# Kernel optimization log

Measured on AMD Instinct MI355X. Metric: run time of the kernel, lower is better.

## Reference

```python
import jax, jax.numpy as jnp
import numpy as np

B, S, D = 4, 2048, 1024
H, HD = 16, 64  # n_heads, head_dim; D == H*HD


def setup_inputs() -> dict:
    key = jax.random.key(0)
    k1, k2, k3, k4, k5 = jax.random.split(key, 5)
    s = 0.02
    return {
        "x": jax.random.normal(k1, (B, S, D), dtype=jnp.float32),
        "w_qkv": jax.random.normal(k2, (D, 3 * D), dtype=jnp.float32) * s,
        "b_qkv": jax.random.normal(k3, (3 * D,), dtype=jnp.float32) * s,
        "w_out": jax.random.normal(k4, (D, D), dtype=jnp.float32) * s,
        "b_out": jax.random.normal(k5, (D,), dtype=jnp.float32) * s,
    }


def reference(x, w_qkv, b_qkv, w_out, b_out):
    b, s, d = x.shape
    qkv = x @ w_qkv + b_qkv                      # [B,S,3D]
    qkv = qkv.reshape(b, s, 3, H, HD)
    qkv = jnp.transpose(qkv, (2, 0, 3, 1, 4))    # [3,B,H,S,HD]
    q, k, v = qkv[0], qkv[1], qkv[2]
    scale = 1.0 / np.sqrt(HD).astype(np.float32)
    scores = jnp.einsum("bhqd,bhkd->bhqk", q, k) * scale  # [B,H,S,S]
    causal = jnp.tril(jnp.ones((s, s), dtype=bool))
    scores = jnp.where(causal[None, None], scores, -jnp.inf)
    weights = jax.nn.softmax(scores, axis=-1)
    attn = jnp.einsum("bhqk,bhkd->bhqd", weights, v)       # [B,H,S,HD]
    attn = jnp.transpose(attn, (0, 2, 1, 3)).reshape(b, s, d)
    return attn @ w_out + b_out
```

## Files before the change

kernel.cpp:

```cpp
#include <hip/hip_runtime.h>
#include <hip/hip_bf16.h>

#define B_DIM 4
#define S_DIM 2048
#define D_DIM 1024
#define H_DIM 16
#define HD_DIM 64

using bf16 = __hip_bfloat16;
using bf16x8 = __attribute__((ext_vector_type(8))) short;
using f32x4 = __attribute__((ext_vector_type(4))) float;

__device__ inline unsigned short f2bfu(float f) {
    bf16 h = __float2bfloat16(f);
    unsigned short s;
    __builtin_memcpy(&s, &h, 2);
    return s;
}
__device__ inline unsigned int pack2bf(float a, float b) {
    return (unsigned int)f2bfu(a) | ((unsigned int)f2bfu(b) << 16);
}
__device__ inline float exp2_raw(float x) {
    float r;
    asm("v_exp_f32 %0, %1" : "=v"(r) : "v"(x));
    return r;
}

typedef __attribute__((address_space(1))) const void cg_void;
typedef __attribute__((address_space(3))) void lds_void;
__device__ inline void gload_lds16(const void* g, void* l) {
    __builtin_amdgcn_global_load_lds((cg_void*)g, (lds_void*)l, 16, 0, 0);
}

__global__ __launch_bounds__(256) void prep_kernel(const float* __restrict__ x,
                                                   bf16* __restrict__ xb,
                                                   const float* __restrict__ wq,
                                                   bf16* __restrict__ wqT,
                                                   const float* __restrict__ wo,
                                                   bf16* __restrict__ woT) {
    int bid = blockIdx.x;
    int tid = threadIdx.x;
    if (bid < 8192) {
        int i = bid * 256 + tid;
        float4 v = reinterpret_cast<const float4*>(x)[i];
        ushort4 o;
        o.x = f2bfu(v.x); o.y = f2bfu(v.y); o.z = f2bfu(v.z); o.w = f2bfu(v.w);
        reinterpret_cast<ushort4*>(xb)[i] = o;
        return;
    }
    __shared__ float tile[32][33];
    const float* in;
    bf16* out;
    int R, C, bx, by;
    if (bid < 11264) {
        int loc = bid - 8192;
        in = wq; out = wqT; R = D_DIM; C = 3 * D_DIM;
        bx = loc % 96; by = loc / 96;
    } else {
        int loc = bid - 11264;
        in = wo; out = woT; R = D_DIM; C = D_DIM;
        bx = loc % 32; by = loc / 32;
    }
    int tx = tid & 31, ty = tid >> 5;
    int c0 = bx * 32, r0 = by * 32;
#pragma unroll
    for (int i = 0; i < 32; i += 8)
        tile[ty + i][tx] = in[(size_t)(r0 + ty + i) * C + c0 + tx];
    __syncthreads();
#pragma unroll
    for (int i = 0; i < 32; i += 8)
        out[(size_t)(c0 + ty + i) * R + r0 + tx] = __float2bfloat16(tile[tx][ty + i]);
}

#define GEMM_PREAMBLE()                                                        \
    const int K = D_DIM;                                                       \
    __shared__ __align__(16) char smem[65536];                                 \
    int bid3 = blockIdx.x;                                                     \
    int xcd = bid3 & 7;                                                        \
    int inner = bid3 >> 3;                                                     \
    int m0 = ((xcd << 3) | (inner & 7)) * 128;        \
    int n0 = (inner >> 3) * 128;                              \
    int tid = threadIdx.x;                                                     \
    int lane = tid & 63;                                                       \
    int w = tid >> 6;                                                          \
    int wr = w >> 1, wc = w & 1;                                               \
    int lr = lane & 15, lk = lane >> 4;                                        \
    f32x4 acc[4][4] = {};                                                      \
    int sr8 = lane >> 3;                                     \
    int scol = (((lane & 7) * 16) ^ (sr8 << 4)) >> 1;    \
    int wub = w * 1024;                                                        \
    const int rsw = (lr & 7) << 4;                                             \
    const bf16* Arow = A + (size_t)(m0 + w * 8 + sr8) * K + scol;              \
    const bf16* Brow = BT + (size_t)(n0 + w * 8 + sr8) * K + scol;

#define GEMM_STAGE_A(buf, kk)                                                  \
    do {                                                                       \
        char* aa_ = smem + (buf) * 32768;                                      \
        gload_lds16(Arow + (kk), aa_ + wub);                                   \
        gload_lds16(Arow + 32 * 1024 + (kk), aa_ + 4096 + wub);                \
        gload_lds16(Arow + 64 * 1024 + (kk), aa_ + 8192 + wub);                \
        gload_lds16(Arow + 96 * 1024 + (kk), aa_ + 12288 + wub);               \
    } while (0)

#define GEMM_STAGE_B(buf, kk)                                                  \
    do {                                                                       \
        char* bb_ = smem + (buf) * 32768 + 16384;                              \
        gload_lds16(Brow + (kk), bb_ + wub);                                   \
        gload_lds16(Brow + 32 * 1024 + (kk), bb_ + 4096 + wub);                \
        gload_lds16(Brow + 64 * 1024 + (kk), bb_ + 8192 + wub);                \
        gload_lds16(Brow + 96 * 1024 + (kk), bb_ + 12288 + wub);               \
    } while (0)

#define GEMM_MAINLOOP()                                                        \
    const int NT = K / 64;                                             \
    GEMM_STAGE_B(0, 0);                                                        \
    GEMM_STAGE_A(0, 0);                                                        \
    bf16x8 af0[4], af1[4], bf0[4], bf1[4], pa1[4], pb1[4];                     \
    for (int t = 0; t < NT; ++t) {                                             \
        char* as = smem + (t & 1) * 32768;                                     \
        char* bs = as + 16384;                                                 \
              \
        asm volatile("s_waitcnt vmcnt(4)" ::: "memory");                       \
        __builtin_amdgcn_s_barrier();                                          \
        __builtin_amdgcn_sched_barrier(0);                                     \
        _Pragma("unroll")                                                      \
        for (int n = 0; n < 4; ++n) {                                          \
            int rb = (wc * 64 + n * 16 + lr) * 128;                            \
            bf0[n] = *(const bf16x8*)(bs + rb + ((lk * 16) ^ rsw));            \
            bf1[n] = *(const bf16x8*)(bs + rb + ((64 + lk * 16) ^ rsw));       \
        }                                                                      \
        if (t + 1 < NT) GEMM_STAGE_B((t + 1) & 1, (t + 1) * 64);               \
        if (t) {                                                               \
            __builtin_amdgcn_s_setprio(1);                                     \
            _Pragma("unroll")                                                  \
            for (int m = 0; m < 4; ++m)                                        \
                _Pragma("unroll")                                              \
                for (int n = 0; n < 4; ++n)                                    \
                    acc[m][n] = __builtin_amdgcn_mfma_f32_16x16x32_bf16(       \
                        pa1[m], pb1[n], acc[m][n], 0, 0, 0);                   \
            __builtin_amdgcn_s_setprio(0);                                     \
        }                                                                      \
                \
        if (t + 1 < NT) asm volatile("s_waitcnt vmcnt(4)" ::: "memory");       \
        else            asm volatile("s_waitcnt vmcnt(0)" ::: "memory");       \
        __builtin_amdgcn_s_barrier();                                          \
        __builtin_amdgcn_sched_barrier(0);                                     \
        _Pragma("unroll")                                                      \
        for (int m = 0; m < 4; ++m) {                                          \
            int rb = (wr * 64 + m * 16 + lr) * 128;                            \
            af0[m] = *(const bf16x8*)(as + rb + ((lk * 16) ^ rsw));            \
            af1[m] = *(const bf16x8*)(as + rb + ((64 + lk * 16) ^ rsw));       \
        }                                                                      \
        if (t + 1 < NT) GEMM_STAGE_A((t + 1) & 1, (t + 1) * 64);               \
        __builtin_amdgcn_s_setprio(1);                                         \
        _Pragma("unroll")                                                      \
        for (int m = 0; m < 4; ++m)                                            \
            _Pragma("unroll")                                                  \
            for (int n = 0; n < 4; ++n)                                        \
                acc[m][n] = __builtin_amdgcn_mfma_f32_16x16x32_bf16(           \
                    af0[m], bf0[n], acc[m][n], 0, 0, 0);                       \
        __builtin_amdgcn_s_setprio(0);                                         \
        _Pragma("unroll")                                                      \
        for (int m = 0; m < 4; ++m) pa1[m] = af1[m];                           \
        _Pragma("unroll")                                                      \
        for (int n = 0; n < 4; ++n) pb1[n] = bf1[n];                           \
    }                                                                          \
                                              \
    _Pragma("unroll")                                                          \
    for (int m = 0; m < 4; ++m)                                                \
        _Pragma("unroll")                                                      \
        for (int n = 0; n < 4; ++n)                                            \
            acc[m][n] = __builtin_amdgcn_mfma_f32_16x16x32_bf16(               \
                pa1[m], pb1[n], acc[m][n], 0, 0, 0);

__global__ __launch_bounds__(256, 2) void gemm_qkv_kernel(const bf16* __restrict__ A,
                                                          const bf16* __restrict__ BT,
                                                          const float* __restrict__ bias,
                                                          bf16* __restrict__ Qo,
                                                          bf16* __restrict__ Ko,
                                                          bf16* __restrict__ Vt) {
    GEMM_PREAMBLE();
    GEMM_MAINLOOP();
    const float QS = 0.18033688f;
    int third = n0 >> 10;
#pragma unroll
    for (int m = 0; m < 4; ++m) {
        int row = m0 + wr * 64 + m * 16 + lk * 4;
        int b = row >> 11, s = row & 2047;
#pragma unroll
        for (int n = 0; n < 4; ++n) {
            int col = n0 + wc * 64 + n * 16 + lr;
            int rem = col & 1023;
            int h = rem >> 6, hd = rem & 63;
            float bv = bias[col];
            if (third == 0) {
#pragma unroll
                for (int i = 0; i < 4; ++i)
                    Qo[(((size_t)b * H_DIM + h) * S_DIM + s + i) * HD_DIM + hd] =
                        __float2bfloat16((acc[m][n][i] + bv) * QS);
            } else if (third == 1) {
#pragma unroll
                for (int i = 0; i < 4; ++i)
                    Ko[(((size_t)b * H_DIM + h) * S_DIM + s + i) * HD_DIM + hd] =
                        __float2bfloat16(acc[m][n][i] + bv);
            } else {
                uint2 d;
                d.x = pack2bf(acc[m][n][0] + bv, acc[m][n][1] + bv);
                d.y = pack2bf(acc[m][n][2] + bv, acc[m][n][3] + bv);
                *(uint2*)&Vt[(((size_t)b * H_DIM + h) * HD_DIM + hd) * S_DIM + s] = d;
            }
        }
    }
}

__global__ __launch_bounds__(256, 4) void attn_kernel(const bf16* __restrict__ Q,
                                                      const bf16* __restrict__ K,
                                                      const bf16* __restrict__ Vt,
                                                      bf16* __restrict__ Aout) {
    __shared__ __align__(16) char smem[40960];
    int bid = blockIdx.x;
    int bh = bid & 63;
    const int st_tbl[16] = {15, 14, 13, 12, 8, 9, 10, 11, 4, 5, 6, 7, 3, 2, 1, 0};
    int st = st_tbl[bid >> 6];
    int b = bh >> 4, h = bh & 15;
    int w = threadIdx.x >> 6;
    int lane = threadIdx.x & 63;
    int lr = lane & 15, lk = lane >> 4;

    const short* Qs = (const short*)(Q + (size_t)bh * S_DIM * HD_DIM);
    const short* Ks = (const short*)(K + (size_t)bh * S_DIM * HD_DIM);
    const short* Vs = (const short*)(Vt + (size_t)bh * HD_DIM * S_DIM);
    char* pb = smem + 32768 + w * 2048;
    const int sw = (lr & 7) << 4;

    int srow = w * 8 + (lane >> 3);
    int sblk = ((lane & 7) ^ (lane >> 3)) * 8;
    int wub = w * 1024;

    int q0w = st * 128 + w * 32;
    int nt = 2 * st + 2;
    int twl = 2 * st + ((w >> 1) & 1);

    bf16x8 qf[2][2];
#pragma unroll
    for (int qg = 0; qg < 2; ++qg)
#pragma unroll
        for (int c = 0; c < 2; ++c)
            qf[qg][c] = *(const bf16x8*)&Qs[(size_t)(q0w + qg * 16 + lr) * 64 + c * 32 + lk * 8];

    bf16x8 onesv;
#pragma unroll
    for (int z = 0; z < 8; ++z) onesv[z] = (short)0x3F80;

    f32x4 o[4][2] = {};
    f32x4 ol[2] = {};

    gload_lds16(Ks + (size_t)srow * 64 + sblk, smem + wub);
    gload_lds16(Ks + (size_t)(32 + srow) * 64 + sblk, smem + 4096 + wub);
    gload_lds16(Vs + (size_t)srow * S_DIM + sblk, smem + 16384 + wub);
    gload_lds16(Vs + (size_t)(32 + srow) * S_DIM + sblk, smem + 20480 + wub);

    for (int t = 0; t < nt; ++t) {
        int cur = t & 1;
        int kv0 = t * 64;
        __syncthreads();
        if (t + 1 < nt) {
            int kn = kv0 + 64;
            char* kd = smem + (cur ^ 1) * 8192;
            char* vd = smem + 16384 + (cur ^ 1) * 8192;
            gload_lds16(Ks + (size_t)(kn + srow) * 64 + sblk, kd + wub);
            gload_lds16(Ks + (size_t)(kn + 32 + srow) * 64 + sblk, kd + 4096 + wub);
            gload_lds16(Vs + (size_t)srow * S_DIM + kn + sblk, vd + wub);
            gload_lds16(Vs + (size_t)(32 + srow) * S_DIM + kn + sblk, vd + 4096 + wub);
        }
        if (t > twl) continue;
        char* kt = smem + cur * 8192;
        char* vt = smem + 16384 + cur * 8192;
        bool diag = (t == twl);
        int mhi = diag ? ((w & 1) ? 4 : 2) : 4;

        f32x4 s[4][2] = {};
        __builtin_amdgcn_s_setprio(1);
#pragma unroll
        for (int m = 0; m < 4; ++m) {
            if (m >= mhi) continue;
            int rb = (m * 16 + lr) * 128;
            bf16x8 ka = *(const bf16x8*)(kt + rb + ((lk * 16) ^ sw));
            bf16x8 kb2 = *(const bf16x8*)(kt + rb + ((64 + lk * 16) ^ sw));
            s[m][0] = __builtin_amdgcn_mfma_f32_16x16x32_bf16(ka, qf[0][0], s[m][0], 0, 0, 0);
            s[m][0] = __builtin_amdgcn_mfma_f32_16x16x32_bf16(kb2, qf[0][1], s[m][0], 0, 0, 0);
            s[m][1] = __builtin_amdgcn_mfma_f32_16x16x32_bf16(ka, qf[1][0], s[m][1], 0, 0, 0);
            s[m][1] = __builtin_amdgcn_mfma_f32_16x16x32_bf16(kb2, qf[1][1], s[m][1], 0, 0, 0);
        }
        __builtin_amdgcn_s_setprio(0);

        if (kv0 + 63 > q0w) {
#pragma unroll
            for (int m = 0; m < 4; ++m)
#pragma unroll
                for (int qg = 0; qg < 2; ++qg) {
                    int qq = q0w + qg * 16 + lr;
#pragma unroll
                    for (int i = 0; i < 4; ++i)
                        if (kv0 + m * 16 + lk * 4 + i > qq) s[m][qg][i] = -1e30f;
                }
        }

#pragma unroll
        for (int m = 0; m < 4; ++m)
#pragma unroll
            for (int qg = 0; qg < 2; ++qg)
#pragma unroll
                for (int i = 0; i < 4; ++i) s[m][qg][i] = exp2_raw(s[m][qg][i]);

        bf16x8 pf[2][2];
#pragma unroll
        for (int qg = 0; qg < 2; ++qg) {
#pragma unroll
            for (int m = 0; m < 4; ++m) {
                uint2 d;
                d.x = pack2bf(s[m][qg][0], s[m][qg][1]);
                d.y = pack2bf(s[m][qg][2], s[m][qg][3]);
                *(uint2*)(pb + lr * 128 + ((m * 32 + lk * 8) ^ sw)) = d;
            }
            pf[qg][0] = *(const bf16x8*)(pb + lr * 128 + ((lk * 16) ^ sw));
            pf[qg][1] = *(const bf16x8*)(pb + lr * 128 + ((64 + lk * 16) ^ sw));
        }

        __builtin_amdgcn_s_setprio(1);
#pragma unroll
        for (int m = 0; m < 4; ++m) {
            int rb = (m * 16 + lr) * 128;
            bf16x8 va = *(const bf16x8*)(vt + rb + ((lk * 16) ^ sw));
            bf16x8 vb2 = *(const bf16x8*)(vt + rb + ((64 + lk * 16) ^ sw));
            o[m][0] = __builtin_amdgcn_mfma_f32_16x16x32_bf16(va, pf[0][0], o[m][0], 0, 0, 0);
            o[m][0] = __builtin_amdgcn_mfma_f32_16x16x32_bf16(vb2, pf[0][1], o[m][0], 0, 0, 0);
            o[m][1] = __builtin_amdgcn_mfma_f32_16x16x32_bf16(va, pf[1][0], o[m][1], 0, 0, 0);
            o[m][1] = __builtin_amdgcn_mfma_f32_16x16x32_bf16(vb2, pf[1][1], o[m][1], 0, 0, 0);
        }
        ol[0] = __builtin_amdgcn_mfma_f32_16x16x32_bf16(onesv, pf[0][0], ol[0], 0, 0, 0);
        ol[0] = __builtin_amdgcn_mfma_f32_16x16x32_bf16(onesv, pf[0][1], ol[0], 0, 0, 0);
        ol[1] = __builtin_amdgcn_mfma_f32_16x16x32_bf16(onesv, pf[1][0], ol[1], 0, 0, 0);
        ol[1] = __builtin_amdgcn_mfma_f32_16x16x32_bf16(onesv, pf[1][1], ol[1], 0, 0, 0);
        __builtin_amdgcn_s_setprio(0);
    }

    short* op = (short*)Aout;
#pragma unroll
    for (int qg = 0; qg < 2; ++qg) {
        float inv = 1.0f / ol[qg][0];
        size_t orow = ((size_t)b * S_DIM + q0w + qg * 16 + lr) * D_DIM + h * 64;
#pragma unroll
        for (int m = 0; m < 4; ++m) {
            uint2 d;
            d.x = pack2bf(o[m][qg][0] * inv, o[m][qg][1] * inv);
            d.y = pack2bf(o[m][qg][2] * inv, o[m][qg][3] * inv);
            *(uint2*)(op + orow + m * 16 + lk * 4) = d;
        }
    }
}

__global__ __launch_bounds__(256, 2) void gemm_out_kernel(const bf16* __restrict__ A,
                                                          const bf16* __restrict__ BT,
                                                          const float* __restrict__ bias,
                                                          float* __restrict__ Out) {
    GEMM_PREAMBLE();
    GEMM_MAINLOOP();
#pragma unroll
    for (int m = 0; m < 4; ++m) {
        int row = m0 + wr * 64 + m * 16 + lk * 4;
#pragma unroll
        for (int n = 0; n < 4; ++n) {
            int col = n0 + wc * 64 + n * 16 + lr;
            float bv = bias[col];
#pragma unroll
            for (int i = 0; i < 4; ++i)
                Out[(size_t)(row + i) * D_DIM + col] = acc[m][n][i] + bv;
        }
    }
}

extern "C" void kernel_launch(void* const* d_in, const int* in_sizes, int n_in,
                              void* d_out, int out_size, void* d_ws, size_t ws_size,
                              hipStream_t stream) {
    const float* x = (const float*)d_in[0];
    const float* w_qkv = (const float*)d_in[1];
    const float* b_qkv = (const float*)d_in[2];
    const float* w_out = (const float*)d_in[3];
    const float* b_out = (const float*)d_in[4];
    float* out = (float*)d_out;

    char* ws = (char*)d_ws;
    const size_t SZ_X = (size_t)B_DIM * S_DIM * D_DIM * 2;
    const size_t SZ_WQKV = (size_t)D_DIM * 3 * D_DIM * 2;
    const size_t SZ_WOUT = (size_t)D_DIM * D_DIM * 2;
    bf16* xb = (bf16*)(ws);
    bf16* wqkvT = (bf16*)(ws + SZ_X);
    bf16* woutT = (bf16*)(ws + SZ_X + SZ_WQKV);
    bf16* Qb = (bf16*)(ws + SZ_X + SZ_WQKV + SZ_WOUT);
    bf16* Kb = (bf16*)(ws + SZ_X + SZ_WQKV + SZ_WOUT + SZ_X);
    bf16* Vtb = (bf16*)(ws + SZ_X + SZ_WQKV + SZ_WOUT + 2 * SZ_X);

    prep_kernel<<<12288, 256, 0, stream>>>(x, xb, w_qkv, wqkvT, w_out, woutT);
    gemm_qkv_kernel<<<1536, 256, 0, stream>>>(xb, wqkvT, b_qkv, Qb, Kb, Vtb);
    attn_kernel<<<dim3(B_DIM * H_DIM * 16), 256, 0, stream>>>(Qb, Kb, Vtb, xb);
    gemm_out_kernel<<<512, 256, 0, stream>>>(xb, woutT, b_out, out);
}
```

Before: 132.8 us.

## Enlarge GEMM tiles to 256-row blocks with 8 waves and larger LDS buffers

Both projection GEMMs move from 128x128 tiles with 256 threads to 256-row tiles with 512 threads. The QKV GEMM uses 256x192 tiles and the output GEMM uses 256x128 tiles. Staging, swizzle, wait counts and grid mapping are regenerated to match, and the double-buffered LDS grows to about 112 KB and 96 KB. The aim is more operand reuse per byte loaded and fewer redundant global reads. The cost is one block per CU and fewer blocks overall, which may hurt latency hiding and load balance.

Result: no change. 130.3 us (median of 2 runs) (-1.9%).

```diff
diff --git a/kernel.cpp b/kernel.cpp
--- a/kernel.cpp
+++ b/kernel.cpp
@@ -72,124 +72,129 @@
         out[(size_t)(c0 + ty + i) * R + r0 + tx] = __float2bfloat16(tile[tx][ty + i]);
 }
 
-#define GEMM_PREAMBLE()                                                        \
+#define GEMM_PRE(BN_)                                                          \
     const int K = D_DIM;                                                       \
-    __shared__ __align__(16) char smem[65536];                                 \
     int bid3 = blockIdx.x;                                                     \
     int xcd = bid3 & 7;                                                        \
     int inner = bid3 >> 3;                                                     \
-    int m0 = ((xcd << 3) | (inner & 7)) * 128;        \
-    int n0 = (inner >> 3) * 128;                              \
+    int m0 = (xcd * 4 + (inner & 3)) * 256;                                    \
+    int n0 = (inner >> 2) * (BN_);                                             \
     int tid = threadIdx.x;                                                     \
     int lane = tid & 63;                                                       \
     int w = tid >> 6;                                                          \
     int wr = w >> 1, wc = w & 1;                                               \
     int lr = lane & 15, lk = lane >> 4;                                        \
-    f32x4 acc[4][4] = {};                                                      \
-    int sr8 = lane >> 3;                                     \
-    int scol = (((lane & 7) * 16) ^ (sr8 << 4)) >> 1;    \
+    int r = tid >> 3;                                                          \
+    int cs = ((tid & 7) ^ (r & 7)) * 8;                                        \
     int wub = w * 1024;                                                        \
     const int rsw = (lr & 7) << 4;                                             \
-    const bf16* Arow = A + (size_t)(m0 + w * 8 + sr8) * K + scol;              \
-    const bf16* Brow = BT + (size_t)(n0 + w * 8 + sr8) * K + scol;
-
-#define GEMM_STAGE_A(buf, kk)                                                  \
+    const bf16* Ag = A + (size_t)(m0 + r) * K + cs;                            \
+    const bf16* Bg = BT + (size_t)(n0 + r) * K + cs;
+
+#define STAGE_A4(buf, kt, BUF_)                                                \
     do {                                                                       \
-        char* aa_ = smem + (buf) * 32768;                                      \
-        gload_lds16(Arow + (kk), aa_ + wub);                                   \
-        gload_lds16(Arow + 32 * 1024 + (kk), aa_ + 4096 + wub);                \
-        gload_lds16(Arow + 64 * 1024 + (kk), aa_ + 8192 + wub);                \
-        gload_lds16(Arow + 96 * 1024 + (kk), aa_ + 12288 + wub);               \
+        char* d_ = smem + (buf) * (BUF_) + wub;                                \
+        gload_lds16(Ag + (kt) * 64, d_);                                       \
+        gload_lds16(Ag + 64 * 1024 + (kt) * 64, d_ + 8192);                    \
+        gload_lds16(Ag + 128 * 1024 + (kt) * 64, d_ + 16384);                  \
+        gload_lds16(Ag + 192 * 1024 + (kt) * 64, d_ + 24576);                  \
     } while (0)
 
-#define GEMM_STAGE_B(buf, kk)                                                  \
+#define STAGE_B3(buf, kt, BUF_)                                                \
     do {                                                                       \
-        char* bb_ = smem + (buf) * 32768 + 16384;                              \
-        gload_lds16(Brow + (kk), bb_ + wub);                                   \
-        gload_lds16(Brow + 32 * 1024 + (kk), bb_ + 4096 + wub);                \
-        gload_lds16(Brow + 64 * 1024 + (kk), bb_ + 8192 + wub);                \
-        gload_lds16(Brow + 96 * 1024 + (kk), bb_ + 12288 + wub);               \
+        char* d_ = smem + (buf) * (BUF_) + 32768 + wub;                        \
+        gload_lds16(Bg + (kt) * 64, d_);                                       \
+        gload_lds16(Bg + 64 * 1024 + (kt) * 64, d_ + 8192);                    \
+        gload_lds16(Bg + 128 * 1024 + (kt) * 64, d_ + 16384);                  \
     } while (0)
 
-#define GEMM_MAINLOOP()                                                        \
+#define STAGE_B2(buf, kt, BUF_)                                                \
+    do {                                                                       \
+        char* d_ = smem + (buf) * (BUF_) + 32768 + wub;                        \
+        gload_lds16(Bg + (kt) * 64, d_);                                       \
+        gload_lds16(Bg + 64 * 1024 + (kt) * 64, d_ + 8192);                    \
+    } while (0)
+
+#define GEMM_MAIN(NF_, STAGE_B_, BUF_, W0_, W1_)                               \
     const int NT = K / 64;                                             \
-    GEMM_STAGE_B(0, 0);                                                        \
-    GEMM_STAGE_A(0, 0);                                                        \
-    bf16x8 af0[4], af1[4], bf0[4], bf1[4], pa1[4], pb1[4];                     \
+    STAGE_B_(0, 0, BUF_);                                                      \
+    STAGE_A4(0, 0, BUF_);                                                      \
+    bf16x8 af0[4], af1[4], bf0[NF_], bf1[NF_], pa1[4], pb1[NF_];               \
     for (int t = 0; t < NT; ++t) {                                             \
-        char* as = smem + (t & 1) * 32768;                                     \
-        char* bs = as + 16384;                                                 \
-              \
-        asm volatile("s_waitcnt vmcnt(4)" ::: "memory");                       \
+        char* bufb = smem + (t & 1) * (BUF_);                                  \
+        asm volatile("s_waitcnt " W0_ ::: "memory");                           \
         __builtin_amdgcn_s_barrier();                                          \
         __builtin_amdgcn_sched_barrier(0);                                     \
         _Pragma("unroll")                                                      \
-        for (int n = 0; n < 4; ++n) {                                          \
-            int rb = (wc * 64 + n * 16 + lr) * 128;                            \
-            bf0[n] = *(const bf16x8*)(bs + rb + ((lk * 16) ^ rsw));            \
-            bf1[n] = *(const bf16x8*)(bs + rb + ((64 + lk * 16) ^ rsw));       \
+        for (int nf = 0; nf < NF_; ++nf) {                                     \
+            int row = wc * (NF_ * 16) + nf * 16 + lr;                          \
+            char* ba = bufb + 32768 + row * 128;                               \
+            bf0[nf] = *(const bf16x8*)(ba + ((lk * 16) ^ rsw));                \
+            bf1[nf] = *(const bf16x8*)(ba + ((64 + lk * 16) ^ rsw));           \
         }                                                                      \
-        if (t + 1 < NT) GEMM_STAGE_B((t + 1) & 1, (t + 1) * 64);               \
+        if (t + 1 < NT) STAGE_B_((t + 1) & 1, t + 1, BUF_);                    \
         if (t) {                                                               \
             __builtin_amdgcn_s_setprio(1);                                     \
             _Pragma("unroll")                                                  \
-            for (int m = 0; m < 4; ++m)                                        \
+            for (int mf = 0; mf < 4; ++mf)                                     \
                 _Pragma("unroll")                                              \
-                for (int n = 0; n < 4; ++n)                                    \
-                    acc[m][n] = __builtin_amdgcn_mfma_f32_16x16x32_bf16(       \
-                        pa1[m], pb1[n], acc[m][n], 0, 0, 0);                   \
+                for (int nf = 0; nf < NF_; ++nf)                               \
+                    acc[mf][nf] = __builtin_amdgcn_mfma_f32_16x16x32_bf16(     \
+                        pa1[mf], pb1[nf], acc[mf][nf], 0, 0, 0);               \
             __builtin_amdgcn_s_setprio(0);                                     \
         }                                                                      \
-                \
-        if (t + 1 < NT) asm volatile("s_waitcnt vmcnt(4)" ::: "memory");       \
+        if (t + 1 < NT) asm volatile("s_waitcnt " W1_ ::: "memory");           \
         else            asm volatile("s_waitcnt vmcnt(0)" ::: "memory");       \
         __builtin_amdgcn_s_barrier();                                          \
         __builtin_amdgcn_sched_barrier(0);                                     \
         _Pragma("unroll")                                                      \
-        for (int m = 0; m < 4; ++m) {                                          \
-            int rb = (wr * 64 + m * 16 + lr) * 128;                            \
-            af0[m] = *(const bf16x8*)(as + rb + ((lk * 16) ^ rsw));            \
-            af1[m] = *(const bf16x8*)(as + rb + ((64 + lk * 16) ^ rsw));       \
+        for (int mf = 0; mf < 4; ++mf) {                                       \
+            int row = wr * 64 + mf * 16 + lr;                                  \
+            char* aa = bufb + row * 128;                                       \
+            af0[mf] = *(const bf16x8*)(aa + ((lk * 16) ^ rsw));                \
+            af1[mf] = *(const bf16x8*)(aa + ((64 + lk * 16) ^ rsw));           \
         }                                                                      \
-        if (t + 1 < NT) GEMM_STAGE_A((t + 1) & 1, (t + 1) * 64);               \
+        if (t + 1 < NT) STAGE_A4((t + 1) & 1, t + 1, BUF_);                    \
         __builtin_amdgcn_s_setprio(1);                                         \
         _Pragma("unroll")                                                      \
-        for (int m = 0; m < 4; ++m)                                            \
+        for (int mf = 0; mf < 4; ++mf)                                         \
             _Pragma("unroll")                                                  \
-            for (int n = 0; n < 4; ++n)                                        \
-                acc[m][n] = __builtin_amdgcn_mfma_f32_16x16x32_bf16(           \
-                    af0[m], bf0[n], acc[m][n], 0, 0, 0);                       \
+            for (int nf = 0; nf < NF_; ++nf)                                   \
+                acc[mf][nf] = __builtin_amdgcn_mfma_f32_16x16x32_bf16(         \
+                    af0[mf], bf0[nf], acc[mf][nf], 0, 0, 0);                   \
         __builtin_amdgcn_s_setprio(0);                                         \
         _Pragma("unroll")                                                      \
-        for (int m = 0; m < 4; ++m) pa1[m] = af1[m];                           \
-        _Pragma("unroll")                                                      \
-        for (int n = 0; n < 4; ++n) pb1[n] = bf1[n];                           \
+        for (int mf = 0; mf < 4; ++mf) pa1[mf] = af1[mf];                      \
+        _Pragma("unroll")                                                      \
+        for (int nf = 0; nf < NF_; ++nf) pb1[nf] = bf1[nf];                    \
     }                                                                          \
-                                              \
     _Pragma("unroll")                                                          \
-    for (int m = 0; m < 4; ++m)                                                \
-        _Pragma("unroll")                                                      \
-        for (int n = 0; n < 4; ++n)                                            \
-            acc[m][n] = __builtin_amdgcn_mfma_f32_16x16x32_bf16(               \
-                pa1[m], pb1[n], acc[m][n], 0, 0, 0);
-
-__global__ __launch_bounds__(256, 2) void gemm_qkv_kernel(const bf16* __restrict__ A,
+    for (int mf = 0; mf < 4; ++mf)                                             \
+        _Pragma("unroll")                                                      \
+        for (int nf = 0; nf < NF_; ++nf)                                       \
+            acc[mf][nf] = __builtin_amdgcn_mfma_f32_16x16x32_bf16(             \
+                pa1[mf], pb1[nf], acc[mf][nf], 0, 0, 0);
+
+__global__ __launch_bounds__(512, 2) void gemm_qkv_kernel(const bf16* __restrict__ A,
                                                           const bf16* __restrict__ BT,
                                                           const float* __restrict__ bias,
                                                           bf16* __restrict__ Qo,
                                                           bf16* __restrict__ Ko,
                                                           bf16* __restrict__ Vt) {
-    GEMM_PREAMBLE();
-    GEMM_MAINLOOP();
+    __shared__ __align__(16) char smem[114688];
+    f32x4 acc[4][6] = {};
+    GEMM_PRE(192);
+    GEMM_MAIN(6, STAGE_B3, 57344, "vmcnt(4)", "vmcnt(3)");
     const float QS = 0.18033688f;
-    int third = n0 >> 10;
-#pragma unroll
-    for (int m = 0; m < 4; ++m) {
-        int row = m0 + wr * 64 + m * 16 + lk * 4;
+#pragma unroll
+    for (int mf = 0; mf < 4; ++mf) {
+        int row = m0 + wr * 64 + mf * 16 + lk * 4;
         int b = row >> 11, s = row & 2047;
 #pragma unroll
-        for (int n = 0; n < 4; ++n) {
-            int col = n0 + wc * 64 + n * 16 + lr;
+        for (int nf = 0; nf < 6; ++nf) {
+            int cb = n0 + wc * 96 + nf * 16;
+            int third = cb >> 10;
+            int col = cb + lr;
             int rem = col & 1023;
             int h = rem >> 6, hd = rem & 63;
             float bv = bias[col];
@@ -197,16 +202,16 @@
 #pragma unroll
                 for (int i = 0; i < 4; ++i)
                     Qo[(((size_t)b * H_DIM + h) * S_DIM + s + i) * HD_DIM + hd] =
-                        __float2bfloat16((acc[m][n][i] + bv) * QS);
+                        __float2bfloat16((acc[mf][nf][i] + bv) * QS);
             } else if (third == 1) {
 #pragma unroll
                 for (int i = 0; i < 4; ++i)
                     Ko[(((size_t)b * H_DIM + h) * S_DIM + s + i) * HD_DIM + hd] =
-                        __float2bfloat16(acc[m][n][i] + bv);
+                        __float2bfloat16(acc[mf][nf][i] + bv);
             } else {
                 uint2 d;
-                d.x = pack2bf(acc[m][n][0] + bv, acc[m][n][1] + bv);
-                d.y = pack2bf(acc[m][n][2] + bv, acc[m][n][3] + bv);
+                d.x = pack2bf(acc[mf][nf][0] + bv, acc[mf][nf][1] + bv);
+                d.y = pack2bf(acc[mf][nf][2] + bv, acc[mf][nf][3] + bv);
                 *(uint2*)&Vt[(((size_t)b * H_DIM + h) * HD_DIM + hd) * S_DIM + s] = d;
             }
         }
@@ -360,22 +365,24 @@
     }
 }
 
-__global__ __launch_bounds__(256, 2) void gemm_out_kernel(const bf16* __restrict__ A,
+__global__ __launch_bounds__(512, 2) void gemm_out_kernel(const bf16* __restrict__ A,
                                                           const bf16* __restrict__ BT,
                                                           const float* __restrict__ bias,
                                                           float* __restrict__ Out) {
-    GEMM_PREAMBLE();
-    GEMM_MAINLOOP();
-#pragma unroll
-    for (int m = 0; m < 4; ++m) {
-        int row = m0 + wr * 64 + m * 16 + lk * 4;
-#pragma unroll
-        for (int n = 0; n < 4; ++n) {
-            int col = n0 + wc * 64 + n * 16 + lr;
+    __shared__ __align__(16) char smem[98304];
+    f32x4 acc[4][4] = {};
+    GEMM_PRE(128);
+    GEMM_MAIN(4, STAGE_B2, 49152, "vmcnt(4)", "vmcnt(2)");
+#pragma unroll
+    for (int mf = 0; mf < 4; ++mf) {
+        int row = m0 + wr * 64 + mf * 16 + lk * 4;
+#pragma unroll
+        for (int nf = 0; nf < 4; ++nf) {
+            int col = n0 + wc * 64 + nf * 16 + lr;
             float bv = bias[col];
 #pragma unroll
             for (int i = 0; i < 4; ++i)
-                Out[(size_t)(row + i) * D_DIM + col] = acc[m][n][i] + bv;
+                Out[(size_t)(row + i) * D_DIM + col] = acc[mf][nf][i] + bv;
         }
     }
 }
@@ -402,7 +409,7 @@
     bf16* Vtb = (bf16*)(ws + SZ_X + SZ_WQKV + SZ_WOUT + 2 * SZ_X);
 
     prep_kernel<<<12288, 256, 0, stream>>>(x, xb, w_qkv, wqkvT, w_out, woutT);
-    gemm_qkv_kernel<<<1536, 256, 0, stream>>>(xb, wqkvT, b_qkv, Qb, Kb, Vtb);
+    gemm_qkv_kernel<<<512, 512, 0, stream>>>(xb, wqkvT, b_qkv, Qb, Kb, Vtb);
     attn_kernel<<<dim3(B_DIM * H_DIM * 16), 256, 0, stream>>>(Qb, Kb, Vtb, xb);
-    gemm_out_kernel<<<512, 256, 0, stream>>>(xb, woutT, b_out, out);
-}
+    gemm_out_kernel<<<256, 512, 0, stream>>>(xb, woutT, b_out, out);
+}
```
